# Kernel optimization log

Hardware: AMD Instinct MI355X
Metric: run time of the kernel (lower is better)

Reference implementation:

```python
import jax, jax.numpy as jnp
import numpy as np

N, F_IN, HID, HEADS, NC, E, NG = 50000, 128, 64, 4, 8, 800000, 512


def setup_inputs() -> dict:
    key = jax.random.key(0)
    ks = jax.random.split(key, 16)
    x = jax.random.normal(ks[0], (N, F_IN), dtype=jnp.float32)
    # edges with src != dst so every node's incoming set is exactly {neighbors, self-loop}
    dst = jax.random.randint(ks[1], (E,), 0, N, dtype=jnp.int64)
    off = jax.random.randint(ks[2], (E,), 1, N, dtype=jnp.int64)
    src = (dst + off) % N
    edge_index = jnp.stack([src, dst])
    batch = jnp.sort(jax.random.randint(ks[3], (N,), 0, NG, dtype=jnp.int64))
    g = 1.0 / np.sqrt(F_IN)
    W1 = jax.random.uniform(ks[4], (F_IN, HEADS * HID), jnp.float32, -g, g)
    att_src1 = jax.random.normal(ks[5], (HEADS, HID), jnp.float32) * 0.1
    att_dst1 = jax.random.normal(ks[6], (HEADS, HID), jnp.float32) * 0.1
    b1 = jnp.zeros((HEADS * HID,), jnp.float32)
    g2 = 1.0 / np.sqrt(HEADS * HID)
    W2 = jax.random.uniform(ks[7], (HEADS * HID, HID), jnp.float32, -g2, g2)
    att_src2 = jax.random.normal(ks[8], (1, HID), jnp.float32) * 0.1
    att_dst2 = jax.random.normal(ks[9], (1, HID), jnp.float32) * 0.1
    b2 = jnp.zeros((HID,), jnp.float32)
    g3 = 1.0 / np.sqrt(HID)
    lin_w = jax.random.uniform(ks[10], (HID, NC), jnp.float32, -g3, g3)
    lin_b = jnp.zeros((NC,), jnp.float32)
    return dict(x=x, edge_index=edge_index, batch=batch, W1=W1, att_src1=att_src1,
                att_dst1=att_dst1, b1=b1, W2=W2, att_src2=att_src2, att_dst2=att_dst2,
                b2=b2, lin_w=lin_w, lin_b=lin_b)


def gat_layer(x, src, dst, W, att_s, att_d, bias, heads, out_ch):
    # PyG GATConv: h = x @ W, e_ij = LeakyReLU(a_s.h_j + a_d.h_i), softmax over dst groups
    h = (x @ W).reshape(-1, heads, out_ch)                    # [N,H,C]
    a_s = jnp.einsum('nhc,hc->nh', h, att_s)                  # [N,H]
    a_d = jnp.einsum('nhc,hc->nh', h, att_d)
    e = jax.nn.leaky_relu(a_s[src] + a_d[dst], 0.2)           # [Ef,H]
    m = jax.ops.segment_max(e, dst, num_segments=N)           # stable segment softmax
    ex = jnp.exp(e - m[dst])
    s = jax.ops.segment_sum(ex, dst, num_segments=N)
    alpha = ex / (s[dst] + 1e-16)                             # [Ef,H]
    msg = h[src] * alpha[:, :, None]                          # [Ef,H,C]
    out = jax.ops.segment_sum(msg, dst, num_segments=N)       # [N,H,C]
    return out.reshape(-1, heads * out_ch) + bias, alpha


def reference(x, edge_index, batch, W1, att_src1, att_dst1, b1,
              W2, att_src2, att_dst2, b2, lin_w, lin_b):
    loops = jnp.arange(N, dtype=edge_index.dtype)
    src = jnp.concatenate([edge_index[0], loops])             # add self-loops (PyG default)
    dst = jnp.concatenate([edge_index[1], loops])
    h, alpha1 = gat_layer(x, src, dst, W1, att_src1, att_dst1, b1, HEADS, HID)
    h = jax.nn.relu(h)
    # conv2 on edge_index_1 (already has self-loops; PyG remove+add is a no-op here)
    h, alpha2 = gat_layer(h, src, dst, W2, att_src2, att_dst2, b2, 1, HID)
    h = jax.nn.relu(h)
    sums = jax.ops.segment_sum(h, batch, num_segments=NG)     # global_mean_pool
    cnt = jax.ops.segment_sum(jnp.ones((N,), h.dtype), batch, num_segments=NG)
    pooled = sums / jnp.maximum(cnt, 1.0)[:, None]
    # dropout is identity in eval mode
    return pooled @ lin_w + lin_b
```

## Files before the change

### kernel.cpp

```cpp
#include <hip/hip_runtime.h>

#define F_IN 128
#define HID 64
#define HEADS 4
#define NC 8

typedef __bf16 bf16_t;
typedef bf16_t bf16x8 __attribute__((ext_vector_type(8)));
typedef float f32x4 __attribute__((ext_vector_type(4)));

union BF8 { bf16x8 v; ushort u[8]; };


__device__ __forceinline__ ushort f2bf(float f) {
    uint u = __float_as_uint(f);
    return (ushort)((u + 0x7fffu + ((u >> 16) & 1u)) >> 16);
}
__device__ __forceinline__ float bf2f(ushort h) {
    return __uint_as_float(((uint)h) << 16);
}
__device__ __forceinline__ float edgew(float e) {
    e = (e > 0.f) ? e : 0.2f * e;
    return __expf(e);
}

__global__ void k_setup(const float* __restrict__ W1, const float* __restrict__ W2,
                        ushort* __restrict__ w1hi, ushort* __restrict__ w1lo,
                        ushort* __restrict__ w2hi, ushort* __restrict__ w2lo,
                        int* __restrict__ deg, int N, int* __restrict__ counts, int NG) {
    int i = blockIdx.x * blockDim.x + threadIdx.x;
    if (i < N) deg[i] = 1;
    if (i < NG) counts[i] = 0;
    if (i < 128 * 256) {
        int k = i >> 8, n = i & 255;
        int cy = n >> 7, ct = (n >> 4) & 7, c = n & 15, kc = k >> 5, ls = (k >> 3) & 3, j = k & 7;
        size_t off = ((((size_t)cy * 8 + ct) * 4 + kc) * 64 + (ls * 16 + c)) * 8 + j;
        float w = W1[i];
        ushort hi = f2bf(w);
        w1hi[off] = hi; w1lo[off] = f2bf(w - bf2f(hi));
    }
    if (i < 256 * 64) {
        int k = i >> 6, n = i & 63;
        int ct = n >> 4, c = n & 15, kc = k >> 5, ls = (k >> 3) & 3, j = k & 7;
        size_t off = (((size_t)ct * 8 + kc) * 64 + (ls * 16 + c)) * 8 + j;
        float w = W2[i];
        ushort hi = f2bf(w);
        w2hi[off] = hi; w2lo[off] = f2bf(w - bf2f(hi));
    }
}

__global__ void k_count(const int* __restrict__ ei, int E, int* __restrict__ deg,
                        const int* __restrict__ batch, int N, int* __restrict__ counts) {
    int i = blockIdx.x * blockDim.x + threadIdx.x;
    if (i < E) atomicAdd(&deg[ei[E + i]], 1);
    if (i < N) atomicAdd(&counts[batch[i]], 1);
}

__global__ __launch_bounds__(1024) void k_scan_part(const int* __restrict__ v,
                                                    int* __restrict__ excl,
                                                    int* __restrict__ bsum, int n) {
    __shared__ int buf[1024];
    int tid = threadIdx.x;
    int i = blockIdx.x * 1024 + tid;
    int val = (i < n) ? v[i] : 0;
    buf[tid] = val;
    __syncthreads();
    for (int off = 1; off < 1024; off <<= 1) {
        int t = (tid >= off) ? buf[tid - off] : 0;
        __syncthreads();
        buf[tid] += t;
        __syncthreads();
    }
    if (i < n) excl[i] = buf[tid] - val;
    if (tid == 1023) bsum[blockIdx.x] = buf[1023];
}

__global__ __launch_bounds__(1024) void k_scan_small2(const int* __restrict__ bsum,
                                                      int* __restrict__ boff, int nb,
                                                      int* __restrict__ total_out,
                                                      const int* __restrict__ counts,
                                                      int* __restrict__ gstart, int ng) {
    __shared__ int buf[1024];
    int tid = threadIdx.x;
    const int* src = (blockIdx.x == 0) ? bsum : counts;
    int cnt = (blockIdx.x == 0) ? nb : ng;
    int val = (tid < cnt) ? src[tid] : 0;
    buf[tid] = val;
    __syncthreads();
    for (int off = 1; off < 1024; off <<= 1) {
        int t = (tid >= off) ? buf[tid - off] : 0;
        __syncthreads();
        buf[tid] += t;
        __syncthreads();
    }
    if (blockIdx.x == 0) {
        if (tid < cnt) boff[tid] = buf[tid] - val;
        if (tid == 1023) total_out[0] = buf[1023];
    } else {
        if (tid < cnt) gstart[tid] = buf[tid] - val;
        if (tid == 1023) gstart[ng] = buf[1023];
    }
}

__global__ void k_scan_add_self(int* __restrict__ rowstart, const int* __restrict__ boff,
                                int* __restrict__ cursor, int* __restrict__ csr, int n) {
    int i = blockIdx.x * blockDim.x + threadIdx.x;
    if (i < n) {
        int rs = rowstart[i] + boff[i >> 10];
        rowstart[i] = rs;
        csr[rs] = i;
        cursor[i] = 1;
    }
}

__global__ void k_scatter(const int* __restrict__ ei, int E, const int* __restrict__ rowstart,
                          int* __restrict__ cursor, int* __restrict__ csr) {
    int e = blockIdx.x * blockDim.x + threadIdx.x;
    if (e < E) {
        int d = ei[E + e], s = ei[e];
        int pos = atomicAdd(&cursor[d], 1);
        csr[rowstart[d] + pos] = s;
    }
}

__global__ __launch_bounds__(256) void k_gemm1(const float* __restrict__ x,
                                               const ushort* __restrict__ w1hi,
                                               const ushort* __restrict__ w1lo,
                                               const float* __restrict__ atts,
                                               const float* __restrict__ attd,
                                               ushort* __restrict__ h1b,
                                               float* __restrict__ as1, float* __restrict__ ad1,
                                               int N) {
    __shared__ __align__(16) ushort lhi[16384];
    __shared__ __align__(16) ushort llo[16384];
    int tid = threadIdx.x;
    int cy = blockIdx.y;
    {
        float4* dh = (float4*)lhi; const float4* sh = (const float4*)(w1hi + (size_t)cy * 16384);
        float4* dl = (float4*)llo; const float4* sl = (const float4*)(w1lo + (size_t)cy * 16384);
        #pragma unroll
        for (int i = 0; i < 8; i++) {
            dh[tid + i * 256] = sh[tid + i * 256];
            dl[tid + i * 256] = sl[tid + i * 256];
        }
    }
    __syncthreads();
    int w = tid >> 6, l = tid & 63;
    int lc = l & 15, lk = l >> 4;
    int rbase = blockIdx.x * 256 + w * 64;

    f32x4 acc[4][8];
    #pragma unroll
    for (int mt = 0; mt < 4; mt++)
        #pragma unroll
        for (int ct = 0; ct < 8; ct++) acc[mt][ct] = (f32x4){0.f, 0.f, 0.f, 0.f};

    #pragma unroll
    for (int kc = 0; kc < 4; kc++) {
        BF8 ahi[4], alo[4];
        #pragma unroll
        for (int mt = 0; mt < 4; mt++) {
            int row = rbase + mt * 16 + lc;
            float4 v0 = {0.f, 0.f, 0.f, 0.f}, v1 = v0;
            if (row < N) {
                const float* xp = x + (size_t)row * F_IN + kc * 32 + lk * 8;
                v0 = *(const float4*)xp; v1 = *(const float4*)(xp + 4);
            }
            float vals[8] = {v0.x, v0.y, v0.z, v0.w, v1.x, v1.y, v1.z, v1.w};
            #pragma unroll
            for (int j = 0; j < 8; j++) {
                ushort h = f2bf(vals[j]);
                ahi[mt].u[j] = h;
                alo[mt].u[j] = f2bf(vals[j] - bf2f(h));
            }
        }
        #pragma unroll
        for (int ct = 0; ct < 8; ct++) {
            int boff = ((ct * 4 + kc) * 64 + l) * 8;
            bf16x8 bhi = *(const bf16x8*)(lhi + boff);
            bf16x8 blo = *(const bf16x8*)(llo + boff);
            #pragma unroll
            for (int mt = 0; mt < 4; mt++) {
                acc[mt][ct] = __builtin_amdgcn_mfma_f32_16x16x32_bf16(ahi[mt].v, bhi, acc[mt][ct], 0, 0, 0);
                acc[mt][ct] = __builtin_amdgcn_mfma_f32_16x16x32_bf16(alo[mt].v, bhi, acc[mt][ct], 0, 0, 0);
                acc[mt][ct] = __builtin_amdgcn_mfma_f32_16x16x32_bf16(ahi[mt].v, blo, acc[mt][ct], 0, 0, 0);
            }
        }
    }
    #pragma unroll
    for (int mt = 0; mt < 4; mt++) {
        int rowb = rbase + mt * 16 + lk * 4;
        #pragma unroll
        for (int ct = 0; ct < 8; ct++) {
            int col = cy * 128 + ct * 16 + lc;
            #pragma unroll
            for (int r = 0; r < 4; r++) {
                int row = rowb + r;
                if (row < N) h1b[(size_t)row * 256 + col] = f2bf(acc[mt][ct][r]);
            }
        }
        #pragma unroll
        for (int hh = 0; hh < 2; hh++) {
            float s[4] = {0.f, 0.f, 0.f, 0.f}, d[4] = {0.f, 0.f, 0.f, 0.f};
            #pragma unroll
            for (int cq = 0; cq < 4; cq++) {
                int ct = hh * 4 + cq;
                int col = cy * 128 + ct * 16 + lc;
                float av = atts[col], dv = attd[col];
                #pragma unroll
                for (int r = 0; r < 4; r++) { s[r] += acc[mt][ct][r] * av; d[r] += acc[mt][ct][r] * dv; }
            }
            #pragma unroll
            for (int r = 0; r < 4; r++) {
                #pragma unroll
                for (int off = 1; off < 16; off <<= 1) {
                    s[r] += __shfl_xor(s[r], off);
                    d[r] += __shfl_xor(d[r], off);
                }
            }
            if (lc == 0) {
                int head = cy * 2 + hh;
                #pragma unroll
                for (int r = 0; r < 4; r++) {
                    int row = rowb + r;
                    if (row < N) { as1[row * 4 + head] = s[r]; ad1[row * 4 + head] = d[r]; }
                }
            }
        }
    }
}

__global__ __launch_bounds__(256) void k_gemm2(const ushort* __restrict__ xin,
                                               const ushort* __restrict__ w2hi,
                                               const ushort* __restrict__ w2lo,
                                               const float* __restrict__ atts,
                                               const float* __restrict__ attd,
                                               ushort* __restrict__ h2b,
                                               float* __restrict__ as2, float* __restrict__ ad2,
                                               int N) {
    __shared__ __align__(16) ushort lhi[16384];
    __shared__ __align__(16) ushort llo[16384];
    int tid = threadIdx.x;
    {
        float4* dh = (float4*)lhi; const float4* sh = (const float4*)w2hi;
        float4* dl = (float4*)llo; const float4* sl = (const float4*)w2lo;
        #pragma unroll
        for (int i = 0; i < 8; i++) {
            dh[tid + i * 256] = sh[tid + i * 256];
            dl[tid + i * 256] = sl[tid + i * 256];
        }
    }
    __syncthreads();
    int w = tid >> 6, l = tid & 63;
    int lc = l & 15, lk = l >> 4;
    int rbase = blockIdx.x * 256 + w * 64;

    f32x4 acc[4][4];
    #pragma unroll
    for (int mt = 0; mt < 4; mt++)
        #pragma unroll
        for (int ct = 0; ct < 4; ct++) acc[mt][ct] = (f32x4){0.f, 0.f, 0.f, 0.f};

    #pragma unroll
    for (int kc = 0; kc < 8; kc++) {
        BF8 a[4];
        #pragma unroll
        for (int mt = 0; mt < 4; mt++) {
            int row = rbase + mt * 16 + lc;
            if (row < N) {
                a[mt].v = *(const bf16x8*)(xin + (size_t)row * 256 + kc * 32 + lk * 8);
            } else {
                #pragma unroll
                for (int j = 0; j < 8; j++) a[mt].u[j] = 0;
            }
        }
        #pragma unroll
        for (int ct = 0; ct < 4; ct++) {
            int boff = ((ct * 8 + kc) * 64 + l) * 8;
            bf16x8 bhi = *(const bf16x8*)(lhi + boff);
            bf16x8 blo = *(const bf16x8*)(llo + boff);
            #pragma unroll
            for (int mt = 0; mt < 4; mt++) {
                acc[mt][ct] = __builtin_amdgcn_mfma_f32_16x16x32_bf16(a[mt].v, bhi, acc[mt][ct], 0, 0, 0);
                acc[mt][ct] = __builtin_amdgcn_mfma_f32_16x16x32_bf16(a[mt].v, blo, acc[mt][ct], 0, 0, 0);
            }
        }
    }
    #pragma unroll
    for (int mt = 0; mt < 4; mt++) {
        int rowb = rbase + mt * 16 + lk * 4;
        #pragma unroll
        for (int ct = 0; ct < 4; ct++) {
            int col = ct * 16 + lc;
            #pragma unroll
            for (int r = 0; r < 4; r++) {
                int row = rowb + r;
                if (row < N) h2b[(size_t)row * 64 + col] = f2bf(acc[mt][ct][r]);
            }
        }
        float s[4] = {0.f, 0.f, 0.f, 0.f}, d[4] = {0.f, 0.f, 0.f, 0.f};
        #pragma unroll
        for (int ct = 0; ct < 4; ct++) {
            int col = ct * 16 + lc;
            float av = atts[col], dv = attd[col];
            #pragma unroll
            for (int r = 0; r < 4; r++) { s[r] += acc[mt][ct][r] * av; d[r] += acc[mt][ct][r] * dv; }
        }
        #pragma unroll
        for (int r = 0; r < 4; r++) {
            #pragma unroll
            for (int off = 1; off < 16; off <<= 1) {
                s[r] += __shfl_xor(s[r], off);
                d[r] += __shfl_xor(d[r], off);
            }
        }
        if (lc == 0) {
            #pragma unroll
            for (int r = 0; r < 4; r++) {
                int row = rowb + r;
                if (row < N) { as2[row] = s[r]; ad2[row] = d[r]; }
            }
        }
    }
}


__global__ __launch_bounds__(256) void k_agg1(const ushort* __restrict__ h1b,
                                              const float* __restrict__ as, const float* __restrict__ ad,
                                              const int* __restrict__ rowstart, const int* __restrict__ csr,
                                              const float* __restrict__ b1,
                                              ushort* __restrict__ out1b, int N) {
    int n = blockIdx.x * 4 + (threadIdx.x >> 6);
    int lane = threadIdx.x & 63;
    if (n >= N) return;
    int head = lane >> 4;
    int coff = lane * 4;
    float adv = ad[n * 4 + head];
    int beg = rowstart[n], end = rowstart[n + 1];
    float a0 = 0.f, a1 = 0.f, a2 = 0.f, a3 = 0.f, ssum = 0.f;
    int j = beg;
    for (; j + 8 <= end; j += 8) {
        int s[8];
        #pragma unroll
        for (int i = 0; i < 8; i++) s[i] = csr[j + i];
        float e[8];
        #pragma unroll
        for (int i = 0; i < 8; i++) e[i] = as[s[i] * 4 + head];
        ushort4 hv[8];
        #pragma unroll
        for (int i = 0; i < 8; i++) hv[i] = *(const ushort4*)(h1b + (size_t)s[i] * 256 + coff);
        #pragma unroll
        for (int i = 0; i < 8; i++) {
            float wv = edgew(e[i] + adv);
            ssum += wv;
            a0 += wv * bf2f(hv[i].x); a1 += wv * bf2f(hv[i].y);
            a2 += wv * bf2f(hv[i].z); a3 += wv * bf2f(hv[i].w);
        }
    }
    for (; j < end; j++) {
        int s0 = csr[j];
        float wv = edgew(as[s0 * 4 + head] + adv);
        ushort4 v0 = *(const ushort4*)(h1b + (size_t)s0 * 256 + coff);
        ssum += wv;
        a0 += wv * bf2f(v0.x); a1 += wv * bf2f(v0.y);
        a2 += wv * bf2f(v0.z); a3 += wv * bf2f(v0.w);
    }
    float inv = 1.f / ssum;
    float o0 = fmaxf(a0 * inv + b1[coff + 0], 0.f);
    float o1 = fmaxf(a1 * inv + b1[coff + 1], 0.f);
    float o2 = fmaxf(a2 * inv + b1[coff + 2], 0.f);
    float o3 = fmaxf(a3 * inv + b1[coff + 3], 0.f);
    ushort4 o;
    o.x = f2bf(o0); o.y = f2bf(o1); o.z = f2bf(o2); o.w = f2bf(o3);
    *(ushort4*)(out1b + (size_t)n * 256 + coff) = o;
}

__global__ __launch_bounds__(256) void k_agg2(const ushort* __restrict__ h2b,
                                              const float* __restrict__ as, const float* __restrict__ ad,
                                              const int* __restrict__ rowstart, const int* __restrict__ csr,
                                              const float* __restrict__ b2,
                                              float* __restrict__ out2, int N) {
    int n = blockIdx.x * 4 + (threadIdx.x >> 6);
    int lane = threadIdx.x & 63;
    if (n >= N) return;
    float adv = ad[n];
    int beg = rowstart[n], end = rowstart[n + 1];
    float acc = 0.f, ssum = 0.f;
    int j = beg;
    for (; j + 8 <= end; j += 8) {
        int s[8];
        #pragma unroll
        for (int i = 0; i < 8; i++) s[i] = csr[j + i];
        float e[8];
        #pragma unroll
        for (int i = 0; i < 8; i++) e[i] = as[s[i]];
        ushort hv[8];
        #pragma unroll
        for (int i = 0; i < 8; i++) hv[i] = h2b[(size_t)s[i] * 64 + lane];
        #pragma unroll
        for (int i = 0; i < 8; i++) {
            float wv = edgew(e[i] + adv);
            ssum += wv;
            acc += wv * bf2f(hv[i]);
        }
    }
    for (; j < end; j++) {
        int s0 = csr[j];
        float wv = edgew(as[s0] + adv);
        ssum += wv;
        acc += wv * bf2f(h2b[(size_t)s0 * 64 + lane]);
    }
    float o = acc / ssum + b2[lane];
    out2[(size_t)n * 64 + lane] = o > 0.f ? o : 0.f;
}


__global__ __launch_bounds__(64) void k_pool(const float* __restrict__ out2,
                                             const int* __restrict__ gstart,
                                             const float* __restrict__ lin_w,
                                             const float* __restrict__ lin_b,
                                             float* __restrict__ out, int NG) {
    __shared__ float mean[64];
    int g = blockIdx.x;
    int lane = threadIdx.x;
    int beg = gstart[g], end = gstart[g + 1];
    float s = 0.f;
    for (int n = beg; n < end; n++) s += out2[(size_t)n * 64 + lane];
    float cnt = (float)(end - beg);
    mean[lane] = s / fmaxf(cnt, 1.f);
    __syncthreads();
    if (lane < NC) {
        float acc = lin_b[lane];
        #pragma unroll
        for (int c = 0; c < 64; c++) acc += mean[c] * lin_w[c * NC + lane];
        out[g * NC + lane] = acc;
    }
}


extern "C" void kernel_launch(void* const* d_in, const int* in_sizes, int n_in,
                              void* d_out, int out_size, void* d_ws, size_t ws_size,
                              hipStream_t stream) {
    const float* x      = (const float*)d_in[0];
    const int*   ei     = (const int*)d_in[1];
    const int*   batch  = (const int*)d_in[2];
    const float* W1     = (const float*)d_in[3];
    const float* att_s1 = (const float*)d_in[4];
    const float* att_d1 = (const float*)d_in[5];
    const float* b1     = (const float*)d_in[6];
    const float* W2     = (const float*)d_in[7];
    const float* att_s2 = (const float*)d_in[8];
    const float* att_d2 = (const float*)d_in[9];
    const float* b2     = (const float*)d_in[10];
    const float* lin_w  = (const float*)d_in[11];
    const float* lin_b  = (const float*)d_in[12];
    float* out = (float*)d_out;

    const int N  = in_sizes[0] / F_IN;
    const int E  = in_sizes[1] / 2;
    const int NG = out_size / NC;
    const int NE = E + N;
    const int NB = (N + 1023) / 1024;

    char* p = (char*)d_ws;
    auto alloc = [&](size_t bytes) { char* r = p; p += (bytes + 255) & ~(size_t)255; return r; };
    ushort* h1b     = (ushort*)alloc(sizeof(ushort) * (size_t)N * 256);
    ushort* out1b   = (ushort*)alloc(sizeof(ushort) * (size_t)N * 256);
    ushort* h2b     = (ushort*)alloc(sizeof(ushort) * (size_t)N * 64);
    float*  out2    = (float*)alloc(sizeof(float) * (size_t)N * 64);
    float*  as1     = (float*)alloc(sizeof(float) * (size_t)N * 4);
    float*  ad1     = (float*)alloc(sizeof(float) * (size_t)N * 4);
    float*  as2     = (float*)alloc(sizeof(float) * (size_t)N);
    float*  ad2     = (float*)alloc(sizeof(float) * (size_t)N);
    int*    rowstart= (int*)alloc(sizeof(int) * (size_t)(N + 1));
    int*    itmp    = (int*)alloc(sizeof(int) * (size_t)N);
    int*    csr     = (int*)alloc(sizeof(int) * (size_t)NE);
    int*    counts  = (int*)alloc(sizeof(int) * (size_t)NG);
    int*    gstart  = (int*)alloc(sizeof(int) * (size_t)(NG + 1));
    int*    bsum    = (int*)alloc(sizeof(int) * 1024);
    int*    boff    = (int*)alloc(sizeof(int) * 1024);
    ushort* w1hi    = (ushort*)alloc(sizeof(ushort) * 32768);
    ushort* w1lo    = (ushort*)alloc(sizeof(ushort) * 32768);
    ushort* w2hi    = (ushort*)alloc(sizeof(ushort) * 16384);
    ushort* w2lo    = (ushort*)alloc(sizeof(ushort) * 16384);

    int bs = 256;
    k_setup<<<(N + bs - 1) / bs, bs, 0, stream>>>(W1, W2, w1hi, w1lo, w2hi, w2lo,
                                                  itmp, N, counts, NG);
    k_count<<<(E + bs - 1) / bs, bs, 0, stream>>>(ei, E, itmp, batch, N, counts);
    k_scan_part<<<NB, 1024, 0, stream>>>(itmp, rowstart, bsum, N);
    k_scan_small2<<<2, 1024, 0, stream>>>(bsum, boff, NB, rowstart + N, counts, gstart, NG);
    k_scan_add_self<<<(N + 1023) / 1024, 1024, 0, stream>>>(rowstart, boff, itmp, csr, N);
    k_scatter<<<(E + bs - 1) / bs, bs, 0, stream>>>(ei, E, rowstart, itmp, csr);

    k_gemm1<<<dim3((N + 255) / 256, 2), 256, 0, stream>>>(x, w1hi, w1lo, att_s1, att_d1, h1b, as1, ad1, N);
    k_agg1<<<(N + 3) / 4, 256, 0, stream>>>(h1b, as1, ad1, rowstart, csr, b1, out1b, N);

    k_gemm2<<<(N + 255) / 256, 256, 0, stream>>>(out1b, w2hi, w2lo, att_s2, att_d2, h2b, as2, ad2, N);
    k_agg2<<<(N + 3) / 4, 256, 0, stream>>>(h2b, as2, ad2, rowstart, csr, b2, out2, N);

    k_pool<<<NG, 64, 0, stream>>>(out2, gstart, lin_w, lin_b, out, NG);
}
```

Measured before the change: 321.4 us.

## Precompute edge softmax weights, drop W1 lo-split MFMA, widen agg2 loads

Adds two kernels that compute per-edge exp weights and inverse per-node sums once, so the aggregation kernels only gather precomputed weights instead of recomputing exp for every lane. The first GEMM drops the low-bf16 part of W1 and its third MFMA pass, cutting shared memory and matrix work at some cost in accuracy. agg2 is reorganised so each wave processes several edges at once with ushort4 loads and a shuffle reduction. The extra kernels add launches plus writes and reads of per-edge weight arrays.

```diff
diff --git a/kernel.cpp b/kernel.cpp
--- a/kernel.cpp
+++ b/kernel.cpp
@@ -25,7 +25,7 @@
 }
 
 __global__ void k_setup(const float* __restrict__ W1, const float* __restrict__ W2,
-                        ushort* __restrict__ w1hi, ushort* __restrict__ w1lo,
+                        ushort* __restrict__ w1hi,
                         ushort* __restrict__ w2hi, ushort* __restrict__ w2lo,
                         int* __restrict__ deg, int N, int* __restrict__ counts, int NG) {
     int i = blockIdx.x * blockDim.x + threadIdx.x;
@@ -35,9 +35,7 @@
         int k = i >> 8, n = i & 255;
         int cy = n >> 7, ct = (n >> 4) & 7, c = n & 15, kc = k >> 5, ls = (k >> 3) & 3, j = k & 7;
         size_t off = ((((size_t)cy * 8 + ct) * 4 + kc) * 64 + (ls * 16 + c)) * 8 + j;
-        float w = W1[i];
-        ushort hi = f2bf(w);
-        w1hi[off] = hi; w1lo[off] = f2bf(w - bf2f(hi));
+        w1hi[off] = f2bf(W1[i]);
     }
     if (i < 256 * 64) {
         int k = i >> 6, n = i & 63;
@@ -125,24 +123,18 @@
 
 __global__ __launch_bounds__(256) void k_gemm1(const float* __restrict__ x,
                                                const ushort* __restrict__ w1hi,
-                                               const ushort* __restrict__ w1lo,
                                                const float* __restrict__ atts,
                                                const float* __restrict__ attd,
                                                ushort* __restrict__ h1b,
                                                float* __restrict__ as1, float* __restrict__ ad1,
                                                int N) {
     __shared__ __align__(16) ushort lhi[16384];
-    __shared__ __align__(16) ushort llo[16384];
     int tid = threadIdx.x;
     int cy = blockIdx.y;
     {
         float4* dh = (float4*)lhi; const float4* sh = (const float4*)(w1hi + (size_t)cy * 16384);
-        float4* dl = (float4*)llo; const float4* sl = (const float4*)(w1lo + (size_t)cy * 16384);
-        #pragma unroll
-        for (int i = 0; i < 8; i++) {
-            dh[tid + i * 256] = sh[tid + i * 256];
-            dl[tid + i * 256] = sl[tid + i * 256];
-        }
+        #pragma unroll
+        for (int i = 0; i < 8; i++) dh[tid + i * 256] = sh[tid + i * 256];
     }
     __syncthreads();
     int w = tid >> 6, l = tid & 63;
@@ -178,12 +170,10 @@
         for (int ct = 0; ct < 8; ct++) {
             int boff = ((ct * 4 + kc) * 64 + l) * 8;
             bf16x8 bhi = *(const bf16x8*)(lhi + boff);
-            bf16x8 blo = *(const bf16x8*)(llo + boff);
             #pragma unroll
             for (int mt = 0; mt < 4; mt++) {
                 acc[mt][ct] = __builtin_amdgcn_mfma_f32_16x16x32_bf16(ahi[mt].v, bhi, acc[mt][ct], 0, 0, 0);
                 acc[mt][ct] = __builtin_amdgcn_mfma_f32_16x16x32_bf16(alo[mt].v, bhi, acc[mt][ct], 0, 0, 0);
-                acc[mt][ct] = __builtin_amdgcn_mfma_f32_16x16x32_bf16(ahi[mt].v, blo, acc[mt][ct], 0, 0, 0);
             }
         }
     }
@@ -325,8 +315,73 @@
 }
 
 
+__global__ __launch_bounds__(256) void k_edgew1(const int* __restrict__ rowstart,
+                                                const int* __restrict__ csr,
+                                                const float* __restrict__ as1,
+                                                const float* __restrict__ ad1,
+                                                float* __restrict__ w4,
+                                                float* __restrict__ issum1, int N) {
+    int n = blockIdx.x * 4 + (threadIdx.x >> 6);
+    int lane = threadIdx.x & 63;
+    if (n >= N) return;
+    int beg = rowstart[n], end = rowstart[n + 1];
+    float4 adv = *(const float4*)(ad1 + (size_t)n * 4);
+    float s0 = 0.f, s1 = 0.f, s2 = 0.f, s3 = 0.f;
+    for (int jb = beg; jb < end; jb += 64) {
+        int j = jb + lane;
+        if (j < end) {
+            int s = csr[j];
+            float4 av = *(const float4*)(as1 + (size_t)s * 4);
+            float w0 = edgew(av.x + adv.x);
+            float w1 = edgew(av.y + adv.y);
+            float w2 = edgew(av.z + adv.z);
+            float w3 = edgew(av.w + adv.w);
+            float4 wv = {w0, w1, w2, w3};
+            *(float4*)(w4 + (size_t)j * 4) = wv;
+            s0 += w0; s1 += w1; s2 += w2; s3 += w3;
+        }
+    }
+    #pragma unroll
+    for (int off = 32; off > 0; off >>= 1) {
+        s0 += __shfl_xor(s0, off); s1 += __shfl_xor(s1, off);
+        s2 += __shfl_xor(s2, off); s3 += __shfl_xor(s3, off);
+    }
+    if (lane == 0) {
+        float4 iv = {1.f / s0, 1.f / s1, 1.f / s2, 1.f / s3};
+        *(float4*)(issum1 + (size_t)n * 4) = iv;
+    }
+}
+
+__global__ __launch_bounds__(256) void k_edgew2(const int* __restrict__ rowstart,
+                                                const int* __restrict__ csr,
+                                                const float* __restrict__ as2,
+                                                const float* __restrict__ ad2,
+                                                float* __restrict__ w2a,
+                                                float* __restrict__ issum2, int N) {
+    int n = blockIdx.x * 4 + (threadIdx.x >> 6);
+    int lane = threadIdx.x & 63;
+    if (n >= N) return;
+    int beg = rowstart[n], end = rowstart[n + 1];
+    float adv = ad2[n];
+    float ss = 0.f;
+    for (int jb = beg; jb < end; jb += 64) {
+        int j = jb + lane;
+        if (j < end) {
+            int s = csr[j];
+            float w = edgew(as2[s] + adv);
+            w2a[j] = w;
+            ss += w;
+        }
+    }
+    #pragma unroll
+    for (int off = 32; off > 0; off >>= 1) ss += __shfl_xor(ss, off);
+    if (lane == 0) issum2[n] = 1.f / ss;
+}
+
+
 __global__ __launch_bounds__(256) void k_agg1(const ushort* __restrict__ h1b,
-                                              const float* __restrict__ as, const float* __restrict__ ad,
+                                              const float* __restrict__ w4,
+                                              const float* __restrict__ issum1,
                                               const int* __restrict__ rowstart, const int* __restrict__ csr,
                                               const float* __restrict__ b1,
                                               ushort* __restrict__ out1b, int N) {
@@ -335,37 +390,31 @@
     if (n >= N) return;
     int head = lane >> 4;
     int coff = lane * 4;
-    float adv = ad[n * 4 + head];
     int beg = rowstart[n], end = rowstart[n + 1];
-    float a0 = 0.f, a1 = 0.f, a2 = 0.f, a3 = 0.f, ssum = 0.f;
+    float inv = issum1[(size_t)n * 4 + head];
+    float a0 = 0.f, a1 = 0.f, a2 = 0.f, a3 = 0.f;
     int j = beg;
     for (; j + 8 <= end; j += 8) {
-        int s[8];
+        int s[8]; float wv[8]; ushort4 hv[8];
         #pragma unroll
         for (int i = 0; i < 8; i++) s[i] = csr[j + i];
-        float e[8];
-        #pragma unroll
-        for (int i = 0; i < 8; i++) e[i] = as[s[i] * 4 + head];
-        ushort4 hv[8];
+        #pragma unroll
+        for (int i = 0; i < 8; i++) wv[i] = w4[(size_t)(j + i) * 4 + head];
         #pragma unroll
         for (int i = 0; i < 8; i++) hv[i] = *(const ushort4*)(h1b + (size_t)s[i] * 256 + coff);
         #pragma unroll
         for (int i = 0; i < 8; i++) {
-            float wv = edgew(e[i] + adv);
-            ssum += wv;
-            a0 += wv * bf2f(hv[i].x); a1 += wv * bf2f(hv[i].y);
-            a2 += wv * bf2f(hv[i].z); a3 += wv * bf2f(hv[i].w);
+            a0 += wv[i] * bf2f(hv[i].x); a1 += wv[i] * bf2f(hv[i].y);
+            a2 += wv[i] * bf2f(hv[i].z); a3 += wv[i] * bf2f(hv[i].w);
         }
     }
     for (; j < end; j++) {
         int s0 = csr[j];
-        float wv = edgew(as[s0 * 4 + head] + adv);
+        float wv = w4[(size_t)j * 4 + head];
         ushort4 v0 = *(const ushort4*)(h1b + (size_t)s0 * 256 + coff);
-        ssum += wv;
         a0 += wv * bf2f(v0.x); a1 += wv * bf2f(v0.y);
         a2 += wv * bf2f(v0.z); a3 += wv * bf2f(v0.w);
     }
-    float inv = 1.f / ssum;
     float o0 = fmaxf(a0 * inv + b1[coff + 0], 0.f);
     float o1 = fmaxf(a1 * inv + b1[coff + 1], 0.f);
     float o2 = fmaxf(a2 * inv + b1[coff + 2], 0.f);
@@ -376,42 +425,57 @@
 }
 
 __global__ __launch_bounds__(256) void k_agg2(const ushort* __restrict__ h2b,
-                                              const float* __restrict__ as, const float* __restrict__ ad,
+                                              const float* __restrict__ w2a,
+                                              const float* __restrict__ issum2,
                                               const int* __restrict__ rowstart, const int* __restrict__ csr,
                                               const float* __restrict__ b2,
                                               float* __restrict__ out2, int N) {
     int n = blockIdx.x * 4 + (threadIdx.x >> 6);
     int lane = threadIdx.x & 63;
     if (n >= N) return;
-    float adv = ad[n];
+    int g = lane >> 4, li = lane & 15;
+    int coff = li * 4;
     int beg = rowstart[n], end = rowstart[n + 1];
-    float acc = 0.f, ssum = 0.f;
+    float a0 = 0.f, a1 = 0.f, a2 = 0.f, a3 = 0.f;
     int j = beg;
     for (; j + 8 <= end; j += 8) {
-        int s[8];
-        #pragma unroll
-        for (int i = 0; i < 8; i++) s[i] = csr[j + i];
-        float e[8];
-        #pragma unroll
-        for (int i = 0; i < 8; i++) e[i] = as[s[i]];
-        ushort hv[8];
-        #pragma unroll
-        for (int i = 0; i < 8; i++) hv[i] = h2b[(size_t)s[i] * 64 + lane];
-        #pragma unroll
-        for (int i = 0; i < 8; i++) {
-            float wv = edgew(e[i] + adv);
-            ssum += wv;
-            acc += wv * bf2f(hv[i]);
-        }
-    }
-    for (; j < end; j++) {
-        int s0 = csr[j];
-        float wv = edgew(as[s0] + adv);
-        ssum += wv;
-        acc += wv * bf2f(h2b[(size_t)s0 * 64 + lane]);
-    }
-    float o = acc / ssum + b2[lane];
-    out2[(size_t)n * 64 + lane] = o > 0.f ? o : 0.f;
+        int sA = csr[j + g], sB = csr[j + 4 + g];
+        float wA = w2a[j + g], wB = w2a[j + 4 + g];
+        ushort4 hA = *(const ushort4*)(h2b + (size_t)sA * 64 + coff);
+        ushort4 hB = *(const ushort4*)(h2b + (size_t)sB * 64 + coff);
+        a0 += wA * bf2f(hA.x) + wB * bf2f(hB.x);
+        a1 += wA * bf2f(hA.y) + wB * bf2f(hB.y);
+        a2 += wA * bf2f(hA.z) + wB * bf2f(hB.z);
+        a3 += wA * bf2f(hA.w) + wB * bf2f(hB.w);
+    }
+    {
+        int j1 = j + g, j2 = j + 4 + g;
+        if (j1 < end) {
+            int s = csr[j1]; float wv = w2a[j1];
+            ushort4 hv = *(const ushort4*)(h2b + (size_t)s * 64 + coff);
+            a0 += wv * bf2f(hv.x); a1 += wv * bf2f(hv.y);
+            a2 += wv * bf2f(hv.z); a3 += wv * bf2f(hv.w);
+        }
+        if (j2 < end) {
+            int s = csr[j2]; float wv = w2a[j2];
+            ushort4 hv = *(const ushort4*)(h2b + (size_t)s * 64 + coff);
+            a0 += wv * bf2f(hv.x); a1 += wv * bf2f(hv.y);
+            a2 += wv * bf2f(hv.z); a3 += wv * bf2f(hv.w);
+        }
+    }
+    a0 += __shfl_xor(a0, 16); a0 += __shfl_xor(a0, 32);
+    a1 += __shfl_xor(a1, 16); a1 += __shfl_xor(a1, 32);
+    a2 += __shfl_xor(a2, 16); a2 += __shfl_xor(a2, 32);
+    a3 += __shfl_xor(a3, 16); a3 += __shfl_xor(a3, 32);
+    if (g == 0) {
+        float inv = issum2[n];
+        float4 o;
+        o.x = fmaxf(a0 * inv + b2[coff + 0], 0.f);
+        o.y = fmaxf(a1 * inv + b2[coff + 1], 0.f);
+        o.z = fmaxf(a2 * inv + b2[coff + 2], 0.f);
+        o.w = fmaxf(a3 * inv + b2[coff + 3], 0.f);
+        *(float4*)(out2 + (size_t)n * 64 + coff) = o;
+    }
 }
 
 
@@ -472,6 +536,10 @@
     float*  ad1     = (float*)alloc(sizeof(float) * (size_t)N * 4);
     float*  as2     = (float*)alloc(sizeof(float) * (size_t)N);
     float*  ad2     = (float*)alloc(sizeof(float) * (size_t)N);
+    float*  w4      = (float*)alloc(sizeof(float) * (size_t)NE * 4);
+    float*  w2a     = (float*)alloc(sizeof(float) * (size_t)NE);
+    float*  issum1  = (float*)alloc(sizeof(float) * (size_t)N * 4);
+    float*  issum2  = (float*)alloc(sizeof(float) * (size_t)N);
     int*    rowstart= (int*)alloc(sizeof(int) * (size_t)(N + 1));
     int*    itmp    = (int*)alloc(sizeof(int) * (size_t)N);
     int*    csr     = (int*)alloc(sizeof(int) * (size_t)NE);
@@ -480,12 +548,11 @@
     int*    bsum    = (int*)alloc(sizeof(int) * 1024);
     int*    boff    = (int*)alloc(sizeof(int) * 1024);
     ushort* w1hi    = (ushort*)alloc(sizeof(ushort) * 32768);
-    ushort* w1lo    = (ushort*)alloc(sizeof(ushort) * 32768);
     ushort* w2hi    = (ushort*)alloc(sizeof(ushort) * 16384);
     ushort* w2lo    = (ushort*)alloc(sizeof(ushort) * 16384);
 
     int bs = 256;
-    k_setup<<<(N + bs - 1) / bs, bs, 0, stream>>>(W1, W2, w1hi, w1lo, w2hi, w2lo,
+    k_setup<<<(N + bs - 1) / bs, bs, 0, stream>>>(W1, W2, w1hi, w2hi, w2lo,
                                                   itmp, N, counts, NG);
     k_count<<<(E + bs - 1) / bs, bs, 0, stream>>>(ei, E, itmp, batch, N, counts);
     k_scan_part<<<NB, 1024, 0, stream>>>(itmp, rowstart, bsum, N);
@@ -493,11 +560,13 @@
     k_scan_add_self<<<(N + 1023) / 1024, 1024, 0, stream>>>(rowstart, boff, itmp, csr, N);
     k_scatter<<<(E + bs - 1) / bs, bs, 0, stream>>>(ei, E, rowstart, itmp, csr);
 
-    k_gemm1<<<dim3((N + 255) / 256, 2), 256, 0, stream>>>(x, w1hi, w1lo, att_s1, att_d1, h1b, as1, ad1, N);
-    k_agg1<<<(N + 3) / 4, 256, 0, stream>>>(h1b, as1, ad1, rowstart, csr, b1, out1b, N);
+    k_gemm1<<<dim3((N + 255) / 256, 2), 256, 0, stream>>>(x, w1hi, att_s1, att_d1, h1b, as1, ad1, N);
+    k_edgew1<<<(N + 3) / 4, 256, 0, stream>>>(rowstart, csr, as1, ad1, w4, issum1, N);
+    k_agg1<<<(N + 3) / 4, 256, 0, stream>>>(h1b, w4, issum1, rowstart, csr, b1, out1b, N);
 
     k_gemm2<<<(N + 255) / 256, 256, 0, stream>>>(out1b, w2hi, w2lo, att_s2, att_d2, h2b, as2, ad2, N);
-    k_agg2<<<(N + 3) / 4, 256, 0, stream>>>(h2b, as2, ad2, rowstart, csr, b2, out2, N);
+    k_edgew2<<<(N + 3) / 4, 256, 0, stream>>>(rowstart, csr, as2, ad2, w2a, issum2, N);
+    k_agg2<<<(N + 3) / 4, 256, 0, stream>>>(h2b, w2a, issum2, rowstart, csr, b2, out2, N);
 
     k_pool<<<NG, 64, 0, stream>>>(out2, gstart, lin_w, lin_b, out, NG);
 }
```

Result: slower. 327.9 us (+2.0%).
